# Performance work log

Measured on AMD Instinct MI355X. Metric: run time of the kernel, lower is better.

The kernel has to match this reference:

```python
import jax, jax.numpy as jnp
import numpy as np

B, H, KH, D, L = 32, 32, 8, 128, 4096  # batch, q heads, kv heads, head dim, kv len
G = H // KH                             # GQA group size
SCALE = 0.08838834764831845             # head_dim ** -0.5


def setup_inputs() -> dict:
    key = jax.random.key(0)
    ks = jax.random.split(key, 5)
    q = jax.random.normal(ks[0], (B, H, D), jnp.float32)
    k = jax.random.normal(ks[1], (B, KH, D), jnp.float32)
    v = jax.random.normal(ks[2], (B, KH, D), jnp.float32)
    k_cache = jax.random.normal(ks[3], (B * L, KH, D), jnp.float32)
    v_cache = jax.random.normal(ks[4], (B * L, KH, D), jnp.float32)
    # paged slot table: row b lists the flat cache slots holding seq b's tokens
    kv_indices = jnp.arange(B * L, dtype=jnp.int32).reshape(B, L)
    return {"q": q, "k": k, "v": v, "k_cache": k_cache, "v_cache": v_cache,
            "kv_indices": kv_indices}


def reference(q, k, v, k_cache, v_cache, kv_indices):
    # output_kv_indices: slot for the newly generated token of each sequence
    cache_loc = kv_indices[:, -1]
    # set_kv_cache: append new k/v token into the paged pool
    k_cache = k_cache.at[cache_loc].set(k)
    v_cache = v_cache.at[cache_loc].set(v)
    # paged gather of each sequence's cached K/V: [B, L, KH, D]
    k_seq = k_cache[kv_indices]
    v_seq = v_cache[kv_indices]
    # GQA: group q heads per kv head -> [B, KH, G, D]
    qg = q.reshape(B, KH, G, D)
    scores = jnp.einsum('bkgd,blkd->bkgl', qg, k_seq) * SCALE  # [B, KH, G, L]
    p = jax.nn.softmax(scores, axis=-1)
    o = jnp.einsum('bkgl,blkd->bkgd', p, v_seq)                # [B, KH, G, D]
    return o.reshape(B, H * D)
```

## Files before the change

kernel.cpp:

```cpp
#include <hip/hip_runtime.h>
#include <math.h>

#define BB 32
#define HH 32
#define KHH 8
#define DD 128
#define LL 4096
#define GG 4
#define SCALE 0.08838834764831845f

#define NTHREADS 512
#define NW 8
#define ROWS_PER_WAVE (LL / NW)
#define NIT (ROWS_PER_WAVE / 4)

__global__ __launch_bounds__(NTHREADS)
void attn_decode(const float* __restrict__ q,
                 const float* __restrict__ knew,
                 const float* __restrict__ vnew,
                 const float* __restrict__ kc,
                 const float* __restrict__ vc,
                 const int* __restrict__ kvi,
                 float* __restrict__ out) {
  __shared__ int   lds_val[LL];
  __shared__ float o_lds[NW][GG][DD];
  __shared__ float m_lds[NW][GG];
  __shared__ float s_lds[NW][GG];
  __shared__ int   lds_loc[BB];

  const int tid  = threadIdx.x;
  const int b    = blockIdx.x >> 3;
  const int kh   = blockIdx.x & 7;
  const int w    = tid >> 6;
  const int lane = tid & 63;
  const int qid  = lane >> 4;
  const int i16  = lane & 15;

  if (tid < BB) lds_loc[tid] = kvi[tid * LL + (LL - 1)];
  __syncthreads();
  for (int l = tid; l < LL; l += NTHREADS) {
    int idx = kvi[b * LL + l];
    int val = idx;
#pragma unroll
    for (int j = 0; j < BB; ++j)
      if (lds_loc[j] == idx) val = -(j + 1);
    lds_val[l] = val;
  }
  __syncthreads();

  const int khq = kh * GG;
  float qf[GG][8];
#pragma unroll
  for (int g = 0; g < GG; ++g) {
    const float* qp = q + ((size_t)b * HH + (khq + g)) * DD + i16 * 8;
#pragma unroll
    for (int j = 0; j < 8; ++j) qf[g][j] = qp[j];
  }

  float m[GG], s[GG], o[GG][8];
#pragma unroll
  for (int g = 0; g < GG; ++g) {
    m[g] = -INFINITY; s[g] = 0.f;
#pragma unroll
    for (int j = 0; j < 8; ++j) o[g][j] = 0.f;
  }

  const int    base  = w * ROWS_PER_WAVE;
  const size_t khoff = (size_t)kh * DD + i16 * 8;

  auto addr = [&](int it, const float*& kp, const float*& vp) {
    int l   = base + it * 4 + qid;
    int val = lds_val[l];
    int row = (val < 0) ? (-val - 1) : val;
    const float* kb = (val < 0) ? knew : kc;
    const float* vb = (val < 0) ? vnew : vc;
    size_t off = ((size_t)row * (KHH * DD)) + khoff;
    kp = kb + off;
    vp = vb + off;
  };

  const float *kp, *vp;
  addr(0, kp, vp);
  float4 ka  = *(const float4*)kp;
  float4 kb4 = *(const float4*)(kp + 4);
  float4 va  = *(const float4*)vp;
  float4 vb4 = *(const float4*)(vp + 4);

  for (int it = 0; it < NIT; ++it) {
    float4 nka, nkb, nva, nvb;
    if (it + 1 < NIT) {
      const float *nkp, *nvp;
      addr(it + 1, nkp, nvp);
      nka = *(const float4*)nkp;
      nkb = *(const float4*)(nkp + 4);
      nva = *(const float4*)nvp;
      nvb = *(const float4*)(nvp + 4);
    } else {
      nka = ka; nkb = kb4; nva = va; nvb = vb4;
    }

#pragma unroll
    for (int g = 0; g < GG; ++g) {
      float sc = qf[g][0]*ka.x  + qf[g][1]*ka.y  + qf[g][2]*ka.z  + qf[g][3]*ka.w
               + qf[g][4]*kb4.x + qf[g][5]*kb4.y + qf[g][6]*kb4.z + qf[g][7]*kb4.w;
#pragma unroll
      for (int msk = 1; msk < 16; msk <<= 1)
        sc += __shfl_xor(sc, msk);
      sc *= SCALE;

      if (sc > m[g]) {
        float so = __expf(m[g] - sc);
        m[g] = sc;
        s[g] *= so;
#pragma unroll
        for (int j = 0; j < 8; ++j) o[g][j] *= so;
      }
      float p = __expf(sc - m[g]);
      s[g] += p;
      o[g][0] += p * va.x;  o[g][1] += p * va.y;  o[g][2] += p * va.z;  o[g][3] += p * va.w;
      o[g][4] += p * vb4.x; o[g][5] += p * vb4.y; o[g][6] += p * vb4.z; o[g][7] += p * vb4.w;
    }

    ka = nka; kb4 = nkb; va = nva; vb4 = nvb;
  }

#pragma unroll
  for (int g = 0; g < GG; ++g) {
#pragma unroll
    for (int off = 16; off < 64; off <<= 1) {
      float m2 = __shfl_xor(m[g], off);
      float s2 = __shfl_xor(s[g], off);
      float M  = fmaxf(m[g], m2);
      float w1 = __expf(m[g] - M);
      float w2 = __expf(m2 - M);
      s[g] = w1 * s[g] + w2 * s2;
#pragma unroll
      for (int j = 0; j < 8; ++j) {
        float o2 = __shfl_xor(o[g][j], off);
        o[g][j] = w1 * o[g][j] + w2 * o2;
      }
      m[g] = M;
    }
  }

  if (lane < 16) {
#pragma unroll
    for (int g = 0; g < GG; ++g) {
#pragma unroll
      for (int j = 0; j < 8; ++j) o_lds[w][g][i16 * 8 + j] = o[g][j];
      if (lane == 0) { m_lds[w][g] = m[g]; s_lds[w][g] = s[g]; }
    }
  }
  __syncthreads();

  {
    int g = tid >> 7;
    int d = tid & 127;
    float M = -INFINITY;
#pragma unroll
    for (int wv = 0; wv < NW; ++wv) M = fmaxf(M, m_lds[wv][g]);
    float ss = 0.f, oo = 0.f;
#pragma unroll
    for (int wv = 0; wv < NW; ++wv) {
      float wt = __expf(m_lds[wv][g] - M);
      ss += wt * s_lds[wv][g];
      oo += wt * o_lds[wv][g][d];
    }
    out[((size_t)b * HH + (khq + g)) * DD + d] = oo / ss;
  }
}

extern "C" void kernel_launch(void* const* d_in, const int* in_sizes, int n_in,
                              void* d_out, int out_size, void* d_ws, size_t ws_size,
                              hipStream_t stream) {
  const float* q    = (const float*)d_in[0];
  const float* knew = (const float*)d_in[1];
  const float* vnew = (const float*)d_in[2];
  const float* kc   = (const float*)d_in[3];
  const float* vc   = (const float*)d_in[4];
  const int*   kvi  = (const int*)d_in[5];
  float* out = (float*)d_out;

  attn_decode<<<dim3(BB * KHH), dim3(NTHREADS), 0, stream>>>(q, knew, vnew, kc, vc, kvi, out);
}
```

Measured before the change: 189.4 us.

## Deepen KV prefetch to two iterations ahead with nontemporal loads

Restructures the streaming loop so each wave keeps two iterations of K/V rows in flight instead of one, using paired register buffers and a loop unrolled by two. Cache reads now use nontemporal loads, since the K/V data is read once, and launch bounds are set to one block per CU. The aim is to hide more global memory latency in this bandwidth-bound decode kernel, at the cost of higher register pressure and possibly lower occupancy.

New measurement: 192.3 us. Within noise of the previous version (+1.5%).

```diff
diff --git a/kernel.cpp b/kernel.cpp
--- a/kernel.cpp
+++ b/kernel.cpp
@@ -14,7 +14,9 @@
 #define ROWS_PER_WAVE (LL / NW)
 #define NIT (ROWS_PER_WAVE / 4)
 
-__global__ __launch_bounds__(NTHREADS)
+typedef float f4 __attribute__((ext_vector_type(4)));
+
+__global__ __launch_bounds__(NTHREADS, 1)
 void attn_decode(const float* __restrict__ q,
                  const float* __restrict__ knew,
                  const float* __restrict__ vnew,
@@ -79,30 +81,20 @@
     vp = vb + off;
   };
 
-  const float *kp, *vp;
-  addr(0, kp, vp);
-  float4 ka  = *(const float4*)kp;
-  float4 kb4 = *(const float4*)(kp + 4);
-  float4 va  = *(const float4*)vp;
-  float4 vb4 = *(const float4*)(vp + 4);
+  auto loadkv = [&](int it, f4& KA, f4& KB, f4& VA, f4& VB) {
+    const float *kp_, *vp_;
+    addr(it, kp_, vp_);
+    KA = __builtin_nontemporal_load((const f4*)kp_);
+    KB = __builtin_nontemporal_load((const f4*)(kp_ + 4));
+    VA = __builtin_nontemporal_load((const f4*)vp_);
+    VB = __builtin_nontemporal_load((const f4*)(vp_ + 4));
+  };
 
-  for (int it = 0; it < NIT; ++it) {
-    float4 nka, nkb, nva, nvb;
-    if (it + 1 < NIT) {
-      const float *nkp, *nvp;
-      addr(it + 1, nkp, nvp);
-      nka = *(const float4*)nkp;
-      nkb = *(const float4*)(nkp + 4);
-      nva = *(const float4*)nvp;
-      nvb = *(const float4*)(nvp + 4);
-    } else {
-      nka = ka; nkb = kb4; nva = va; nvb = vb4;
-    }
-
+  auto compute = [&](f4 ka, f4 kb4, f4 va, f4 vb4) {
 #pragma unroll
     for (int g = 0; g < GG; ++g) {
-      float sc = qf[g][0]*ka.x  + qf[g][1]*ka.y  + qf[g][2]*ka.z  + qf[g][3]*ka.w
-               + qf[g][4]*kb4.x + qf[g][5]*kb4.y + qf[g][6]*kb4.z + qf[g][7]*kb4.w;
+      float sc = qf[g][0]*ka[0]  + qf[g][1]*ka[1]  + qf[g][2]*ka[2]  + qf[g][3]*ka[3]
+               + qf[g][4]*kb4[0] + qf[g][5]*kb4[1] + qf[g][6]*kb4[2] + qf[g][7]*kb4[3];
 #pragma unroll
       for (int msk = 1; msk < 16; msk <<= 1)
         sc += __shfl_xor(sc, msk);
@@ -117,11 +109,27 @@
       }
       float p = __expf(sc - m[g]);
       s[g] += p;
-      o[g][0] += p * va.x;  o[g][1] += p * va.y;  o[g][2] += p * va.z;  o[g][3] += p * va.w;
-      o[g][4] += p * vb4.x; o[g][5] += p * vb4.y; o[g][6] += p * vb4.z; o[g][7] += p * vb4.w;
+      o[g][0] += p * va[0];  o[g][1] += p * va[1];  o[g][2] += p * va[2];  o[g][3] += p * va[3];
+      o[g][4] += p * vb4[0]; o[g][5] += p * vb4[1]; o[g][6] += p * vb4[2]; o[g][7] += p * vb4[3];
     }
+  };
 
-    ka = nka; kb4 = nkb; va = nva; vb4 = nvb;
+  f4 kaA = {0}, kbA = {0}, vaA = {0}, vbA = {0};
+  f4 kaB = {0}, kbB = {0}, vaB = {0}, vbB = {0};
+  f4 kaC = {0}, kbC = {0}, vaC = {0}, vbC = {0};
+  f4 kaD = {0}, kbD = {0}, vaD = {0}, vbD = {0};
+
+  loadkv(0, kaA, kbA, vaA, vbA);
+  loadkv(1, kaB, kbB, vaB, vbB);
+
+#pragma unroll 1
+  for (int it = 0; it < NIT; it += 2) {
+    if (it + 2 < NIT) loadkv(it + 2, kaC, kbC, vaC, vbC);
+    compute(kaA, kbA, vaA, vbA);
+    if (it + 3 < NIT) loadkv(it + 3, kaD, kbD, vaD, vbD);
+    compute(kaB, kbB, vaB, vbB);
+    kaA = kaC; kbA = kbC; vaA = vaC; vbA = vbC;
+    kaB = kaD; kbB = kbD; vaB = vaD; vbB = vbD;
   }
 
 #pragma unroll
```
